# Kernel tuning notes

Measured on AMD Instinct MI355X. Metric: run time of the kernel, lower is better.

## Reference

```python
import jax, jax.numpy as jnp
import numpy as np

K = 81  # num_classes + 1 background
CH = [512, 1024, 512, 256, 256, 256]          # per-level feature channels
MBOX = [4, 6, 6, 6, 4, 4]                     # default boxes per location
# extra layers: (out_ch, in_ch, kernel, stride, pad), per _make_extra_layers for SSD300
EXTRA = [(256, 1024, 1, 1, 0), (512, 256, 3, 2, 1),
         (128, 512, 1, 1, 0), (256, 128, 3, 2, 1),
         (128, 256, 1, 1, 0), (256, 128, 3, 1, 0),
         (128, 256, 1, 1, 0), (256, 128, 3, 1, 0)]


def _conv(x, w, b, s, p):
    y = jax.lax.conv_general_dilated(x, w, (s, s), [(p, p), (p, p)],
                                     dimension_numbers=('NCHW', 'OIHW', 'NCHW'))
    return y + b[None, :, None, None]


def setup_inputs() -> dict:
    key = jax.random.key(0)
    ks = iter(jax.random.split(key, 64))
    d = {}
    d['feat0'] = jax.random.normal(next(ks), (16, 512, 38, 38), jnp.float32)
    d['feat1'] = jax.random.normal(next(ks), (16, 1024, 19, 19), jnp.float32)
    d['l2norm_w'] = jnp.full((512,), 20.0, jnp.float32)  # init constant = l2norm_scale
    for i, (o, ci, k, s, p) in enumerate(EXTRA):
        d[f'e{i}_w'] = jax.random.normal(next(ks), (o, ci, k, k), jnp.float32) / np.sqrt(ci * k * k)
        d[f'e{i}_b'] = jnp.zeros((o,), jnp.float32)
    for i, (c, m) in enumerate(zip(CH, MBOX)):
        sc = 1.0 / np.sqrt(c * 9)
        d[f'cls{i}_w'] = jax.random.normal(next(ks), (m * K, c, 3, 3), jnp.float32) * sc
        d[f'cls{i}_b'] = jnp.zeros((m * K,), jnp.float32)
        d[f'box{i}_w'] = jax.random.normal(next(ks), (m * 4, c, 3, 3), jnp.float32) * sc
        d[f'box{i}_b'] = jnp.zeros((m * 4,), jnp.float32)
    return d


def _forward(feat0, feat1, l2norm_w, extra_params, head_params):
    # L2Norm on conv4_3
    norm = jnp.sqrt(jnp.sum(feat0 * feat0, axis=1, keepdims=True)) + 1e-10
    f0 = l2norm_w[None, :, None, None] * feat0 / norm
    features = [f0, feat1]
    x = feat1
    for idx, ((w, b), (_, _, k, s, p)) in enumerate(zip(extra_params, EXTRA)):
        x = jax.nn.relu(_conv(x, w, b, s, p))
        if idx % 2 == 1:
            features.append(x)
    confs, locs = [], []
    for f, (cw, cb, bw, bb) in zip(features, head_params):
        n = f.shape[0]
        # (N, m*K, H, W) -> (N, H, W, m*K) -> (N, H*W*m, K)
        confs.append(_conv(f, cw, cb, 1, 1).transpose(0, 2, 3, 1).reshape(n, -1, K))
        locs.append(_conv(f, bw, bb, 1, 1).transpose(0, 2, 3, 1).reshape(n, -1, 4))
    conf = jnp.concatenate(confs, axis=1)  # (N, 8732, 81)
    loc = jnp.concatenate(locs, axis=1)    # (N, 8732, 4)
    return jnp.concatenate([conf, loc], axis=-1)  # packed (N, 8732, 85)


def reference(feat0, feat1, l2norm_w,
              e0_w, e0_b, e1_w, e1_b, e2_w, e2_b, e3_w, e3_b,
              e4_w, e4_b, e5_w, e5_b, e6_w, e6_b, e7_w, e7_b,
              cls0_w, cls0_b, box0_w, box0_b,
              cls1_w, cls1_b, box1_w, box1_b,
              cls2_w, cls2_b, box2_w, box2_b,
              cls3_w, cls3_b, box3_w, box3_b,
              cls4_w, cls4_b, box4_w, box4_b,
              cls5_w, cls5_b, box5_w, box5_b):
    extra_params = [(e0_w, e0_b), (e1_w, e1_b), (e2_w, e2_b), (e3_w, e3_b),
                    (e4_w, e4_b), (e5_w, e5_b), (e6_w, e6_b), (e7_w, e7_b)]
    head_params = [(cls0_w, cls0_b, box0_w, box0_b), (cls1_w, cls1_b, box1_w, box1_b),
                   (cls2_w, cls2_b, box2_w, box2_b), (cls3_w, cls3_b, box3_w, box3_b),
                   (cls4_w, cls4_b, box4_w, box4_b), (cls5_w, cls5_b, box5_w, box5_b)]
    return _forward(feat0, feat1, l2norm_w, extra_params, head_params)
```

## Files before the change

kernel.cpp:

```cpp
#include <hip/hip_runtime.h>
#include <hip/hip_bf16.h>

typedef __attribute__((ext_vector_type(8))) short short8;
typedef __attribute__((ext_vector_type(4))) float f32x4;

__device__ __forceinline__ short f2bf(float f) {
  unsigned u = __float_as_uint(f);
  u += 0x7fffu + ((u >> 16) & 1u);
  return (short)(u >> 16);
}

__device__ __forceinline__ void gload16(const short* g, short* l) {
  __builtin_amdgcn_global_load_lds(
      (const __attribute__((address_space(1))) unsigned int*)g,
      (__attribute__((address_space(3))) unsigned int*)l, 16, 0, 0);
}

__global__ __launch_bounds__(256) void f0prep_kernel(const float* __restrict__ src,
    short* __restrict__ dst, const float* __restrict__ l2w,
    int H, int W, int Wp, int nstride, int hh) {
  constexpr int C = 512;
  __shared__ float red[8][32];
  __shared__ float sscale[32];
  __shared__ float tile[32][33];
  int n = blockIdx.z;
  int P = H * W;
  int p0 = blockIdx.x * 32;
  int pl = threadIdx.x & 31, cg = threadIdx.x >> 5;
  const float* s = src + (size_t)n * C * P;
  float ss = 0.f;
  int p = p0 + pl;
  if (p < P) {
    for (int k = 0; k < 64; ++k) {
      float v = s[(size_t)(cg * 64 + k) * P + p];
      ss += v * v;
    }
  }
  red[cg][pl] = ss;
  __syncthreads();
  if (threadIdx.x < 32) {
    float tot = 0.f;
    #pragma unroll
    for (int g = 0; g < 8; ++g) tot += red[g][threadIdx.x];
    sscale[threadIdx.x] = 1.0f / (sqrtf(tot) + 1e-10f);
  }
  __syncthreads();
  for (int ct = 0; ct < 16; ++ct) {
    int c0 = ct * 32;
    __syncthreads();
    #pragma unroll
    for (int i = 0; i < 4; ++i) {
      int cl = cg + i * 8;
      tile[cl][pl] = (p < P) ? s[(size_t)(c0 + cl) * P + p] : 0.f;
    }
    __syncthreads();
    #pragma unroll
    for (int i = 0; i < 4; ++i) {
      int pll = cg + i * 8;
      int pp = p0 + pll;
      if (pp >= P) continue;
      int c = c0 + pl;
      float v = tile[pl][pll] * l2w[c] * sscale[pll];
      int y = pp / W, x = pp - y * W;
      dst[((size_t)n * nstride + (y + hh) * Wp + (x + hh)) * C + c] = f2bf(v);
    }
  }
}

__global__ __launch_bounds__(256) void to_nhwc_kernel(const float* __restrict__ src,
    short* __restrict__ dst, int C, int H, int W, int Wp, int nstride, int hh) {
  __shared__ float tile[32][33];
  int n = blockIdx.z;
  int P = H * W;
  int p0 = blockIdx.x * 32, c0 = blockIdx.y * 32;
  int tp = threadIdx.x & 31, tr = threadIdx.x >> 5;
  const float* s = src + (size_t)n * C * P;
  #pragma unroll
  for (int i = 0; i < 4; ++i) {
    int cl = tr + i * 8;
    int p = p0 + tp;
    tile[cl][tp] = (p < P) ? s[(size_t)(c0 + cl) * P + p] : 0.f;
  }
  __syncthreads();
  #pragma unroll
  for (int i = 0; i < 4; ++i) {
    int pl = tr + i * 8;
    int p = p0 + pl;
    if (p >= P) continue;
    int c = c0 + tp;
    float v = tile[tp][pl];
    int y = p / W, x = p - y * W;
    dst[((size_t)n * nstride + (y + hh) * Wp + (x + hh)) * C + c] = f2bf(v);
  }
}

struct WSeg { const float* src; short* dst; int Ci; int S; int elems; };
struct WPrep { WSeg seg[20]; };

__global__ __launch_bounds__(256) void wprep_kernel(WPrep p, int total) {
  int i = blockIdx.x * 256 + threadIdx.x;
  if (i >= total) return;
  int local = i;
  int si = 0;
  while (local >= p.seg[si].elems) { local -= p.seg[si].elems; ++si; }
  WSeg sg = p.seg[si];
  int ci = local % sg.Ci;
  int q  = local / sg.Ci;
  int s  = q % sg.S;
  int co = q / sg.S;
  float v = sg.src[((size_t)co * sg.Ci + ci) * sg.S + s];
  sg.dst[local] = f2bf(v);
}

struct ConvP {
  const short* in;
  const short* w;
  const float* b1;
  const float* b2;
  short* out_bf;
  float* out_f;
  int M, Ci, iHp, iWp, Ho, Wo, Co;
  int S, kdim, stride, ioff;
  int oWp, onstride, oh;
  int mbox, row_base;
};

template<int BM, int BN, int BK, int WM, int WN, bool HEAD>
__device__ __forceinline__ void conv_core(const ConvP p, int bx, int by) {
  constexpr int NT  = WM * WN * 64;
  constexpr int CPR = BK / 8;
  constexpr int RPP = NT / CPR;
  constexpr int NRA = BM / RPP, NRB = BN / RPP;
  constexpr int AM = BM / WM / 16, AN = BN / WN / 16, KK = BK / 32;
  constexpr int ABUF = BM * BK, BBUF = BN * BK;
  __shared__ short As[2 * ABUF];
  __shared__ short Bs[2 * BBUF];
  const int t = threadIdx.x, lane = t & 63, wave = t >> 6;
  const int HW = p.Ho * p.Wo;
  const int sr = t / CPR;
  const int slot = ((t & (CPR - 1)) ^ (sr & (CPR - 1))) * 8;

  const short* aBase[NRA];
  const short* bBase[NRB];
  #pragma unroll
  for (int i = 0; i < NRA; ++i) {
    int pos = bx * BM + sr + i * RPP; if (pos >= p.M) pos = p.M - 1;
    int n = pos / HW, rem = pos - n * HW;
    int yo = rem / p.Wo, xo = rem - yo * p.Wo;
    aBase[i] = p.in + ((size_t)(n * p.iHp + yo * p.stride + p.ioff) * p.iWp
                      + xo * p.stride + p.ioff) * p.Ci + slot;
  }
  #pragma unroll
  for (int i = 0; i < NRB; ++i) {
    int co = by * BN + sr + i * RPP; if (co >= p.Co) co = p.Co - 1;
    bBase[i] = p.w + (size_t)co * p.S * p.Ci + slot;
  }
  const int cs = p.Ci / BK;
  const int total = p.S * cs;

  auto stage = [&](int buf, int aoff, int boff) {
    #pragma unroll
    for (int i = 0; i < NRA; ++i)
      gload16(aBase[i] + aoff, &As[buf * ABUF + i * (NT * 8) + t * 8]);
    #pragma unroll
    for (int i = 0; i < NRB; ++i)
      gload16(bBase[i] + boff, &Bs[buf * BBUF + i * (NT * 8) + t * 8]);
  };

  int ntap = 0, ncc = 0;
  auto aoff_cur = [&]() -> int {
    if (p.S == 1) return ncc * BK;
    unsigned dy = (unsigned)ntap / 3u;
    int dx = ntap - (int)dy * 3;
    return ((int)dy * p.iWp + dx) * p.Ci + ncc * BK;
  };

  stage(0, aoff_cur(), 0);
  ++ncc; if (ncc == cs) { ncc = 0; ++ntap; }
  __syncthreads();

  f32x4 acc[AM][AN];
  #pragma unroll
  for (int i = 0; i < AM; ++i)
    #pragma unroll
    for (int j = 0; j < AN; ++j)
      acc[i][j] = (f32x4){0.f, 0.f, 0.f, 0.f};

  const int wr = (wave / WN) * (BM / WM), wc = (wave % WN) * (BN / WN);
  const int lrow = lane & 15, kgrp = lane >> 4;

  int cur = 0;
  for (int ks = 0; ks < total; ++ks) {
    if (ks + 1 < total) {
      stage(cur ^ 1, aoff_cur(), (ks + 1) * BK);
      ++ncc; if (ncc == cs) { ncc = 0; ++ntap; }
    }
    const short* aRd0 = &As[cur * ABUF];
    const short* bRd0 = &Bs[cur * BBUF];
    short8 a[AM][KK], b[AN][KK];
    #pragma unroll
    for (int i = 0; i < AM; ++i) {
      int r = wr + i * 16 + lrow;
      #pragma unroll
      for (int kk = 0; kk < KK; ++kk) {
        int ch = ((kk << 2) | kgrp) ^ (r & (CPR - 1));
        a[i][kk] = *reinterpret_cast<const short8*>(aRd0 + r * BK + ch * 8);
      }
    }
    #pragma unroll
    for (int j = 0; j < AN; ++j) {
      int r = wc + j * 16 + lrow;
      #pragma unroll
      for (int kk = 0; kk < KK; ++kk) {
        int ch = ((kk << 2) | kgrp) ^ (r & (CPR - 1));
        b[j][kk] = *reinterpret_cast<const short8*>(bRd0 + r * BK + ch * 8);
      }
    }
    #pragma unroll
    for (int kk = 0; kk < KK; ++kk)
      #pragma unroll
      for (int i = 0; i < AM; ++i)
        #pragma unroll
        for (int j = 0; j < AN; ++j)
          acc[i][j] = __builtin_amdgcn_mfma_f32_16x16x32_bf16(a[i][kk], b[j][kk], acc[i][j], 0, 0, 0);
    __syncthreads();
    cur ^= 1;
  }

  const int mk = p.mbox * 81;
  const int rb_ = (lane >> 4) * 4, cl_ = lane & 15;
  #pragma unroll
  for (int i = 0; i < AM; ++i)
    #pragma unroll
    for (int j = 0; j < AN; ++j)
      #pragma unroll
      for (int q = 0; q < 4; ++q) {
        int po = bx * BM + wr + i * 16 + rb_ + q;
        int co = by * BN + wc + j * 16 + cl_;
        if (po >= p.M || co >= p.Co) continue;
        float v = acc[i][j][q];
        if (!HEAD) {
          int n2 = po / HW, sp = po - n2 * HW;
          int y = sp / p.Wo, x = sp - y * p.Wo;
          float v2 = fmaxf(v + p.b1[co], 0.f);
          p.out_bf[((size_t)n2 * p.onstride + (y + p.oh) * p.oWp + (x + p.oh)) * p.Co + co] = f2bf(v2);
        } else {
          int n2 = po / HW, sp = po - n2 * HW;
          int mi, col; float bias;
          if (co < mk) { mi = co / 81; col = co - mi * 81; bias = p.b1[co]; }
          else { int cbx = co - mk; mi = cbx >> 2; col = 81 + (cbx & 3); bias = p.b2[cbx]; }
          size_t orow = (size_t)n2 * 8732 + p.row_base + (size_t)sp * p.mbox + mi;
          p.out_f[orow * 85 + col] = v + bias;
        }
      }
}

__global__ __launch_bounds__(256) void conv_tile64(ConvP p) {
  conv_core<64, 64, 128, 2, 2, false>(p, blockIdx.x, blockIdx.y);
}

struct HeadPack { ConvP L[6]; int g0[6]; int nbyA[6]; int sb[56]; };

__global__ __launch_bounds__(512) void head_grouped(HeadPack h) {
  int p = blockIdx.x, x = p & 7, s = p >> 3;
  if (s >= h.sb[48 + x]) return;
  int li = 0;
  #pragma unroll
  for (int i = 1; i < 6; ++i) if (s >= h.sb[i * 8 + x]) li = i;
  int r = s - h.sb[li * 8 + x];
  int nby = h.nbyA[li];
  int k = r / nby, by = r - k * nby;
  int bx = ((x - h.g0[li]) & 7) + 8 * k;
  conv_core<128, 128, 64, 2, 4, true>(h.L[li], bx, by);
}

extern "C" void kernel_launch(void* const* d_in, const int* in_sizes, int n_in,
                              void* d_out, int out_size, void* d_ws, size_t ws_size,
                              hipStream_t stream) {
  const float* feat0 = (const float*)d_in[0];
  const float* feat1 = (const float*)d_in[1];
  const float* l2w   = (const float*)d_in[2];
  const float* ew[8]; const float* eb[8];
  for (int i = 0; i < 8; ++i) { ew[i] = (const float*)d_in[3 + 2 * i]; eb[i] = (const float*)d_in[4 + 2 * i]; }
  const float* cw[6]; const float* cb[6]; const float* bw[6]; const float* bb[6];
  for (int i = 0; i < 6; ++i) {
    cw[i] = (const float*)d_in[19 + 4 * i]; cb[i] = (const float*)d_in[20 + 4 * i];
    bw[i] = (const float*)d_in[21 + 4 * i]; bb[i] = (const float*)d_in[22 + 4 * i];
  }
  float* out = (float*)d_out;
  char* ws = (char*)d_ws;
  size_t off = 0;
  auto alloc = [&](size_t bytes) -> char* {
    char* p = ws + off;
    off = (off + bytes + 255) & ~(size_t)255;
    return p;
  };
  char* featStart = ws + off;
  short* f0b = (short*)alloc((size_t)16 * 40 * 40 * 512 * 2);
  short* f1b = (short*)alloc((size_t)16 * 21 * 21 * 1024 * 2);
  short* xe0 = (short*)alloc((size_t)16 * 21 * 21 * 256 * 2);
  short* f2b = (short*)alloc((size_t)16 * 12 * 12 * 512 * 2);
  short* xe2 = (short*)alloc((size_t)16 * 12 * 12 * 128 * 2);
  short* f3b = (short*)alloc((size_t)16 * 7 * 7 * 256 * 2);
  short* xe4 = (short*)alloc((size_t)16 * 5 * 5 * 128 * 2);
  short* f4b = (short*)alloc((size_t)16 * 5 * 5 * 256 * 2);
  short* xe6 = (short*)alloc((size_t)16 * 3 * 3 * 128 * 2);
  short* f5b = (short*)alloc((size_t)16 * 3 * 3 * 256 * 2);
  size_t featBytes = (size_t)((ws + off) - featStart);

  static const int eCo[8] = {256, 512, 128, 256, 128, 256, 128, 256};
  static const int eCi[8] = {1024, 256, 512, 128, 256, 128, 256, 128};
  static const int eS[8]  = {1, 9, 1, 9, 1, 9, 1, 9};
  static const int mbox[6] = {4, 6, 6, 6, 4, 4};
  static const int hCi[6] = {512, 1024, 512, 256, 256, 256};

  WPrep wp; int total = 0; int segi = 0;
  short* ewb[8]; short* hwb[6];
  for (int i = 0; i < 8; ++i) {
    int e = eCo[i] * eCi[i] * eS[i];
    ewb[i] = (short*)alloc((size_t)e * 2);
    wp.seg[segi++] = {ew[i], ewb[i], eCi[i], eS[i], e};
    total += e;
  }
  for (int L = 0; L < 6; ++L) {
    int co = mbox[L] * 85;
    int e = co * hCi[L] * 9;
    hwb[L] = (short*)alloc((size_t)e * 2);
    int ecls = mbox[L] * 81 * hCi[L] * 9;
    wp.seg[segi++] = {cw[L], hwb[L], hCi[L], 9, ecls};
    wp.seg[segi++] = {bw[L], hwb[L] + (size_t)mbox[L] * 81 * 9 * hCi[L], hCi[L], 9, e - ecls};
    total += e;
  }

  hipMemsetAsync(featStart, 0, featBytes, stream);
  f0prep_kernel<<<dim3(46, 1, 16), 256, 0, stream>>>(feat0, f0b, l2w, 38, 38, 40, 1600, 1);
  to_nhwc_kernel<<<dim3(12, 32, 16), 256, 0, stream>>>(feat1, f1b, 1024, 19, 19, 21, 441, 1);
  wprep_kernel<<<dim3((total + 255) / 256), 256, 0, stream>>>(wp, total);

  auto mkP = [&](const short* in, const short* wbuf, const float* b1, const float* b2,
                 short* outb, float* outf, int Ci, int iHp, int iWp, int Ho, int Wo,
                 int Co, int S, int kd, int st, int ioff, int oWp, int onstride, int oh,
                 int m, int rb) {
    ConvP p{}; p.in = in; p.w = wbuf; p.b1 = b1; p.b2 = b2; p.out_bf = outb; p.out_f = outf;
    p.M = 16 * Ho * Wo; p.Ci = Ci; p.iHp = iHp; p.iWp = iWp; p.Ho = Ho; p.Wo = Wo; p.Co = Co;
    p.S = S; p.kdim = kd; p.stride = st; p.ioff = ioff;
    p.oWp = oWp; p.onstride = onstride; p.oh = oh; p.mbox = m; p.row_base = rb;
    return p;
  };
  auto run64 = [&](ConvP p) {
    conv_tile64<<<dim3((p.M + 63) / 64, (p.Co + 63) / 64), 256, 0, stream>>>(p);
  };

  run64(mkP(f1b, ewb[0], eb[0], nullptr, xe0, nullptr, 1024, 21, 21, 19, 19, 256, 1, 1, 1, 1, 21, 441, 1, 0, 0));
  run64(mkP(xe0, ewb[1], eb[1], nullptr, f2b, nullptr,  256, 21, 21, 10, 10, 512, 9, 3, 2, 0, 12, 144, 1, 0, 0));
  run64(mkP(f2b, ewb[2], eb[2], nullptr, xe2, nullptr,  512, 12, 12, 10, 10, 128, 1, 1, 1, 1, 12, 144, 1, 0, 0));
  run64(mkP(xe2, ewb[3], eb[3], nullptr, f3b, nullptr,  128, 12, 12,  5,  5, 256, 9, 3, 2, 0,  7,  49, 1, 0, 0));
  run64(mkP(f3b, ewb[4], eb[4], nullptr, xe4, nullptr,  256,  7,  7,  5,  5, 128, 1, 1, 1, 1,  5,  25, 0, 0, 0));
  run64(mkP(xe4, ewb[5], eb[5], nullptr, f4b, nullptr,  128,  5,  5,  3,  3, 256, 9, 3, 1, 0,  5,  25, 1, 0, 0));
  run64(mkP(f4b, ewb[6], eb[6], nullptr, xe6, nullptr,  256,  5,  5,  3,  3, 128, 1, 1, 1, 1,  3,   9, 0, 0, 0));
  run64(mkP(xe6, ewb[7], eb[7], nullptr, f5b, nullptr,  128,  3,  3,  1,  1, 256, 9, 3, 1, 0,  3,   9, 1, 0, 0));

  HeadPack h;
  h.L[0] = mkP(f1b, hwb[1], cb[1], bb[1], nullptr, out, 1024, 21, 21, 19, 19, 6 * 85, 9, 3, 1, 0, 0, 0, 0, 6, 5776);
  h.L[1] = mkP(f0b, hwb[0], cb[0], bb[0], nullptr, out,  512, 40, 40, 38, 38, 4 * 85, 9, 3, 1, 0, 0, 0, 0, 4, 0);
  h.L[2] = mkP(f2b, hwb[2], cb[2], bb[2], nullptr, out,  512, 12, 12, 10, 10, 6 * 85, 9, 3, 1, 0, 0, 0, 0, 6, 7942);
  h.L[3] = mkP(f3b, hwb[3], cb[3], bb[3], nullptr, out,  256,  7,  7,  5,  5, 6 * 85, 9, 3, 1, 0, 0, 0, 0, 6, 8542);
  h.L[4] = mkP(f4b, hwb[4], cb[4], bb[4], nullptr, out,  256,  5,  5,  3,  3, 4 * 85, 9, 3, 1, 0, 0, 0, 0, 4, 8692);
  h.L[5] = mkP(f5b, hwb[5], cb[5], bb[5], nullptr, out,  256,  3,  3,  1,  1, 4 * 85, 9, 3, 1, 0, 0, 0, 0, 4, 8728);

  int gid = 0;
  for (int x = 0; x < 8; ++x) h.sb[x] = 0;
  for (int li = 0; li < 6; ++li) {
    int nbx = (h.L[li].M + 127) / 128;
    h.nbyA[li] = (h.L[li].Co + 127) / 128;
    h.g0[li] = gid & 7;
    for (int x = 0; x < 8; ++x) {
      int f = ((x - gid) % 8 + 8) % 8;
      int cnt = (f < nbx) ? (nbx - f + 7) / 8 : 0;
      h.sb[(li + 1) * 8 + x] = h.sb[li * 8 + x] + h.nbyA[li] * cnt;
    }
    gid += nbx;
  }
  int maxSlots = 0;
  for (int x = 0; x < 8; ++x) if (h.sb[48 + x] > maxSlots) maxSlots = h.sb[48 + x];
  head_grouped<<<dim3(8 * maxSlots), 512, 0, stream>>>(h);
}
```

Before: 383.3 us.

## Fuse extra-layer chain and heads into one persistent mega kernel with grid barriers

Replaces the eight separate extra-layer conv launches and the grouped head launch with a single kernel. The first 128 blocks run the extra-layer chain persistently, synchronising between layers with atomic-counter grid barriers, and then compute the four small head levels. The remaining blocks compute the two large head levels concurrently with the chain. This removes launch gaps and tail idle time and overlaps the dependent chain with the big head work. The risks are possible deadlock if the 128 chain blocks are not all co-resident, spin-wait overhead, and the chain tile now using 512 threads.

```diff
diff --git a/kernel.cpp b/kernel.cpp
--- a/kernel.cpp
+++ b/kernel.cpp
@@ -126,15 +126,15 @@
 };
 
 template<int BM, int BN, int BK, int WM, int WN, bool HEAD>
-__device__ __forceinline__ void conv_core(const ConvP p, int bx, int by) {
+__device__ __forceinline__ void conv_core(const ConvP p, int bx, int by, short* smem) {
   constexpr int NT  = WM * WN * 64;
   constexpr int CPR = BK / 8;
   constexpr int RPP = NT / CPR;
   constexpr int NRA = BM / RPP, NRB = BN / RPP;
   constexpr int AM = BM / WM / 16, AN = BN / WN / 16, KK = BK / 32;
   constexpr int ABUF = BM * BK, BBUF = BN * BK;
-  __shared__ short As[2 * ABUF];
-  __shared__ short Bs[2 * BBUF];
+  short* As = smem;
+  short* Bs = smem + 2 * ABUF;
   const int t = threadIdx.x, lane = t & 63, wave = t >> 6;
   const int HW = p.Ho * p.Wo;
   const int sr = t / CPR;
@@ -255,23 +255,56 @@
       }
 }
 
-__global__ __launch_bounds__(256) void conv_tile64(ConvP p) {
-  conv_core<64, 64, 128, 2, 2, false>(p, blockIdx.x, blockIdx.y);
-}
-
-struct HeadPack { ConvP L[6]; int g0[6]; int nbyA[6]; int sb[56]; };
-
-__global__ __launch_bounds__(512) void head_grouped(HeadPack h) {
-  int p = blockIdx.x, x = p & 7, s = p >> 3;
-  if (s >= h.sb[48 + x]) return;
-  int li = 0;
-  #pragma unroll
-  for (int i = 1; i < 6; ++i) if (s >= h.sb[i * 8 + x]) li = i;
-  int r = s - h.sb[li * 8 + x];
-  int nby = h.nbyA[li];
-  int k = r / nby, by = r - k * nby;
-  int bx = ((x - h.g0[li]) & 7) + 8 * k;
-  conv_core<128, 128, 64, 2, 4, true>(h.L[li], bx, by);
+struct ChainPhase { ConvP p; int nbx, nblk; };
+struct SmallHead { ConvP p; int nbx, base; };
+struct MegaPack {
+  ConvP big[2]; int bg0[2]; int bnby[2]; int bsb[24];
+  ChainPhase ch[8];
+  SmallHead sh[4];
+  int nSmallBlk;
+  int nChain;
+};
+
+__global__ __launch_bounds__(512) void mega_kernel(MegaPack m, unsigned* cnt) {
+  __shared__ short smem[32768];
+  int bid = blockIdx.x;
+  if (bid >= m.nChain) {
+    int hid = bid - m.nChain;
+    int x = hid & 7, s = hid >> 3;
+    if (s >= m.bsb[16 + x]) return;
+    int li = (s >= m.bsb[8 + x]) ? 1 : 0;
+    int r = s - m.bsb[li * 8 + x];
+    int nby = m.bnby[li];
+    int k = r / nby, by = r - k * nby;
+    int bx = ((x - m.bg0[li]) & 7) + 8 * k;
+    conv_core<128, 128, 64, 2, 4, true>(m.big[li], bx, by, smem);
+    return;
+  }
+  int cb = bid;
+  for (int ph = 0; ph < 8; ++ph) {
+    for (int idx = cb; idx < m.ch[ph].nblk; idx += m.nChain) {
+      int bx = idx % m.ch[ph].nbx, by = idx / m.ch[ph].nbx;
+      conv_core<64, 64, 128, 2, 4, false>(m.ch[ph].p, bx, by, smem);
+    }
+    __threadfence();
+    __syncthreads();
+    if (threadIdx.x == 0) {
+      atomicAdd(&cnt[ph], 1u);
+      while (__hip_atomic_load(&cnt[ph], __ATOMIC_ACQUIRE, __HIP_MEMORY_SCOPE_AGENT)
+             < (unsigned)m.nChain)
+        __builtin_amdgcn_s_sleep(2);
+    }
+    __syncthreads();
+    __threadfence();
+  }
+  for (int idx = cb; idx < m.nSmallBlk; idx += m.nChain) {
+    int li = 0;
+    #pragma unroll
+    for (int i = 1; i < 4; ++i) if (idx >= m.sh[i].base) li = i;
+    int local = idx - m.sh[li].base;
+    int bx = local % m.sh[li].nbx, by = local / m.sh[li].nbx;
+    conv_core<64, 64, 128, 2, 4, true>(m.sh[li].p, bx, by, smem);
+  }
 }
 
 extern "C" void kernel_launch(void* const* d_in, const int* in_sizes, int n_in,
@@ -295,6 +328,7 @@
     off = (off + bytes + 255) & ~(size_t)255;
     return p;
   };
+  unsigned* cnt = (unsigned*)alloc(32);
   char* featStart = ws + off;
   short* f0b = (short*)alloc((size_t)16 * 40 * 40 * 512 * 2);
   short* f1b = (short*)alloc((size_t)16 * 21 * 21 * 1024 * 2);
@@ -332,6 +366,7 @@
     total += e;
   }
 
+  hipMemsetAsync(cnt, 0, 32, stream);
   hipMemsetAsync(featStart, 0, featBytes, stream);
   f0prep_kernel<<<dim3(46, 1, 16), 256, 0, stream>>>(feat0, f0b, l2w, 38, 38, 40, 1600, 1);
   to_nhwc_kernel<<<dim3(12, 32, 16), 256, 0, stream>>>(feat1, f1b, 1024, 19, 19, 21, 441, 1);
@@ -347,41 +382,57 @@
     p.oWp = oWp; p.onstride = onstride; p.oh = oh; p.mbox = m; p.row_base = rb;
     return p;
   };
-  auto run64 = [&](ConvP p) {
-    conv_tile64<<<dim3((p.M + 63) / 64, (p.Co + 63) / 64), 256, 0, stream>>>(p);
-  };
-
-  run64(mkP(f1b, ewb[0], eb[0], nullptr, xe0, nullptr, 1024, 21, 21, 19, 19, 256, 1, 1, 1, 1, 21, 441, 1, 0, 0));
-  run64(mkP(xe0, ewb[1], eb[1], nullptr, f2b, nullptr,  256, 21, 21, 10, 10, 512, 9, 3, 2, 0, 12, 144, 1, 0, 0));
-  run64(mkP(f2b, ewb[2], eb[2], nullptr, xe2, nullptr,  512, 12, 12, 10, 10, 128, 1, 1, 1, 1, 12, 144, 1, 0, 0));
-  run64(mkP(xe2, ewb[3], eb[3], nullptr, f3b, nullptr,  128, 12, 12,  5,  5, 256, 9, 3, 2, 0,  7,  49, 1, 0, 0));
-  run64(mkP(f3b, ewb[4], eb[4], nullptr, xe4, nullptr,  256,  7,  7,  5,  5, 128, 1, 1, 1, 1,  5,  25, 0, 0, 0));
-  run64(mkP(xe4, ewb[5], eb[5], nullptr, f4b, nullptr,  128,  5,  5,  3,  3, 256, 9, 3, 1, 0,  5,  25, 1, 0, 0));
-  run64(mkP(f4b, ewb[6], eb[6], nullptr, xe6, nullptr,  256,  5,  5,  3,  3, 128, 1, 1, 1, 1,  3,   9, 0, 0, 0));
-  run64(mkP(xe6, ewb[7], eb[7], nullptr, f5b, nullptr,  128,  3,  3,  1,  1, 256, 9, 3, 1, 0,  3,   9, 1, 0, 0));
-
-  HeadPack h;
-  h.L[0] = mkP(f1b, hwb[1], cb[1], bb[1], nullptr, out, 1024, 21, 21, 19, 19, 6 * 85, 9, 3, 1, 0, 0, 0, 0, 6, 5776);
-  h.L[1] = mkP(f0b, hwb[0], cb[0], bb[0], nullptr, out,  512, 40, 40, 38, 38, 4 * 85, 9, 3, 1, 0, 0, 0, 0, 4, 0);
-  h.L[2] = mkP(f2b, hwb[2], cb[2], bb[2], nullptr, out,  512, 12, 12, 10, 10, 6 * 85, 9, 3, 1, 0, 0, 0, 0, 6, 7942);
-  h.L[3] = mkP(f3b, hwb[3], cb[3], bb[3], nullptr, out,  256,  7,  7,  5,  5, 6 * 85, 9, 3, 1, 0, 0, 0, 0, 6, 8542);
-  h.L[4] = mkP(f4b, hwb[4], cb[4], bb[4], nullptr, out,  256,  5,  5,  3,  3, 4 * 85, 9, 3, 1, 0, 0, 0, 0, 4, 8692);
-  h.L[5] = mkP(f5b, hwb[5], cb[5], bb[5], nullptr, out,  256,  3,  3,  1,  1, 4 * 85, 9, 3, 1, 0, 0, 0, 0, 4, 8728);
-
-  int gid = 0;
-  for (int x = 0; x < 8; ++x) h.sb[x] = 0;
-  for (int li = 0; li < 6; ++li) {
-    int nbx = (h.L[li].M + 127) / 128;
-    h.nbyA[li] = (h.L[li].Co + 127) / 128;
-    h.g0[li] = gid & 7;
-    for (int x = 0; x < 8; ++x) {
-      int f = ((x - gid) % 8 + 8) % 8;
-      int cnt = (f < nbx) ? (nbx - f + 7) / 8 : 0;
-      h.sb[(li + 1) * 8 + x] = h.sb[li * 8 + x] + h.nbyA[li] * cnt;
-    }
-    gid += nbx;
+
+  MegaPack m;
+  m.nChain = 128;
+  ConvP ep[8];
+  ep[0] = mkP(f1b, ewb[0], eb[0], nullptr, xe0, nullptr, 1024, 21, 21, 19, 19, 256, 1, 1, 1, 1, 21, 441, 1, 0, 0);
+  ep[1] = mkP(xe0, ewb[1], eb[1], nullptr, f2b, nullptr,  256, 21, 21, 10, 10, 512, 9, 3, 2, 0, 12, 144, 1, 0, 0);
+  ep[2] = mkP(f2b, ewb[2], eb[2], nullptr, xe2, nullptr,  512, 12, 12, 10, 10, 128, 1, 1, 1, 1, 12, 144, 1, 0, 0);
+  ep[3] = mkP(xe2, ewb[3], eb[3], nullptr, f3b, nullptr,  128, 12, 12,  5,  5, 256, 9, 3, 2, 0,  7,  49, 1, 0, 0);
+  ep[4] = mkP(f3b, ewb[4], eb[4], nullptr, xe4, nullptr,  256,  7,  7,  5,  5, 128, 1, 1, 1, 1,  5,  25, 0, 0, 0);
+  ep[5] = mkP(xe4, ewb[5], eb[5], nullptr, f4b, nullptr,  128,  5,  5,  3,  3, 256, 9, 3, 1, 0,  5,  25, 1, 0, 0);
+  ep[6] = mkP(f4b, ewb[6], eb[6], nullptr, xe6, nullptr,  256,  5,  5,  3,  3, 128, 1, 1, 1, 1,  3,   9, 0, 0, 0);
+  ep[7] = mkP(xe6, ewb[7], eb[7], nullptr, f5b, nullptr,  128,  3,  3,  1,  1, 256, 9, 3, 1, 0,  3,   9, 1, 0, 0);
+  for (int i = 0; i < 8; ++i) {
+    m.ch[i].p = ep[i];
+    m.ch[i].nbx = (ep[i].M + 63) / 64;
+    m.ch[i].nblk = m.ch[i].nbx * ((ep[i].Co + 63) / 64);
+  }
+  m.big[0] = mkP(f1b, hwb[1], cb[1], bb[1], nullptr, out, 1024, 21, 21, 19, 19, 6 * 85, 9, 3, 1, 0, 0, 0, 0, 6, 5776);
+  m.big[1] = mkP(f0b, hwb[0], cb[0], bb[0], nullptr, out,  512, 40, 40, 38, 38, 4 * 85, 9, 3, 1, 0, 0, 0, 0, 4, 0);
+  ConvP sp[4];
+  sp[0] = mkP(f2b, hwb[2], cb[2], bb[2], nullptr, out, 512, 12, 12, 10, 10, 6 * 85, 9, 3, 1, 0, 0, 0, 0, 6, 7942);
+  sp[1] = mkP(f3b, hwb[3], cb[3], bb[3], nullptr, out, 256,  7,  7,  5,  5, 6 * 85, 9, 3, 1, 0, 0, 0, 0, 6, 8542);
+  sp[2] = mkP(f4b, hwb[4], cb[4], bb[4], nullptr, out, 256,  5,  5,  3,  3, 4 * 85, 9, 3, 1, 0, 0, 0, 0, 4, 8692);
+  sp[3] = mkP(f5b, hwb[5], cb[5], bb[5], nullptr, out, 256,  3,  3,  1,  1, 4 * 85, 9, 3, 1, 0, 0, 0, 0, 4, 8728);
+  {
+    int base = 0;
+    for (int i = 0; i < 4; ++i) {
+      m.sh[i].p = sp[i];
+      m.sh[i].nbx = (sp[i].M + 63) / 64;
+      m.sh[i].base = base;
+      base += m.sh[i].nbx * ((sp[i].Co + 63) / 64);
+    }
+    m.nSmallBlk = base;
+  }
+  {
+    int gid = 0;
+    for (int x = 0; x < 8; ++x) m.bsb[x] = 0;
+    for (int li = 0; li < 2; ++li) {
+      int nbx = (m.big[li].M + 127) / 128;
+      m.bnby[li] = (m.big[li].Co + 127) / 128;
+      m.bg0[li] = gid & 7;
+      for (int x = 0; x < 8; ++x) {
+        int f = ((x - gid) % 8 + 8) % 8;
+        int c = (f < nbx) ? (nbx - f + 7) / 8 : 0;
+        m.bsb[(li + 1) * 8 + x] = m.bsb[li * 8 + x] + m.bnby[li] * c;
+      }
+      gid += nbx;
+    }
   }
   int maxSlots = 0;
-  for (int x = 0; x < 8; ++x) if (h.sb[48 + x] > maxSlots) maxSlots = h.sb[48 + x];
-  head_grouped<<<dim3(8 * maxSlots), 512, 0, stream>>>(h);
-}
+  for (int x = 0; x < 8; ++x) if (m.bsb[16 + x] > maxSlots) maxSlots = m.bsb[16 + x];
+  int grid = m.nChain + 8 * maxSlots;
+  mega_kernel<<<dim3(grid), 512, 0, stream>>>(m, cnt);
+}
```

Result: slower. 946.8 us (+147.0%).
